# Performance work log

Measured on AMD Instinct MI355X. Metric: run time of the kernel, lower is better.

## Reference

```python
import jax, jax.numpy as jnp
import numpy as np

B, S, H, NH = 4, 2048, 1024, 16
HS = H // NH  # head size 64


def setup_inputs() -> dict:
    key = jax.random.key(0)
    ks = jax.random.split(key, 12)
    inv = 1.0 / np.sqrt(H)
    d = {
        "query": jax.random.normal(ks[0], (B, S, H), jnp.float32),
        "key": jax.random.normal(ks[1], (B, S, H), jnp.float32),
        "value": jax.random.normal(ks[2], (B, S, H), jnp.float32),
        "causal_mask": jnp.tril(jnp.ones((S, S), dtype=bool)),
        "Wq": jax.random.uniform(ks[3], (H, H), jnp.float32, -inv, inv),
        "bq": jax.random.uniform(ks[4], (H,), jnp.float32, -inv, inv),
        "Wk": jax.random.uniform(ks[5], (H, H), jnp.float32, -inv, inv),
        "bk": jax.random.uniform(ks[6], (H,), jnp.float32, -inv, inv),
        "Wv": jax.random.uniform(ks[7], (H, H), jnp.float32, -inv, inv),
        "bv": jax.random.uniform(ks[8], (H,), jnp.float32, -inv, inv),
        "Wo": jax.random.uniform(ks[9], (H, H), jnp.float32, -inv, inv),
        "bo": jax.random.uniform(ks[10], (H,), jnp.float32, -inv, inv),
    }
    return d


def reference(query, key, value, causal_mask, Wq, bq, Wk, bk, Wv, bv, Wo, bo):
    # Linear projections (torch Linear: x @ W.T + b)
    q = query @ Wq.T + bq
    k = key @ Wk.T + bk
    v = value @ Wv.T + bv
    # [B, NH, S, HS]
    q = q.reshape(B, S, NH, HS).transpose(0, 2, 1, 3)
    k = k.reshape(B, S, NH, HS).transpose(0, 2, 1, 3)
    v = v.reshape(B, S, NH, HS).transpose(0, 2, 1, 3)
    scores = jnp.einsum("bhqd,bhkd->bhqk", q, k) / jnp.sqrt(jnp.float32(HS))
    scores = jnp.where(causal_mask[None, None, :, :], scores, -jnp.inf)
    attn = jax.nn.softmax(scores, axis=-1)
    ctx = jnp.einsum("bhqk,bhkd->bhqd", attn, v)
    ctx = ctx.transpose(0, 2, 1, 3).reshape(B, S, H)
    return ctx @ Wo.T + bo
```

## Files before the change

### kernel.cpp

```cpp
#include <hip/hip_runtime.h>
#include <hip/hip_bf16.h>
#include <math.h>

#define B_  4
#define S_  2048
#define H_  1024
#define NH_ 16
#define HS_ 64

typedef __attribute__((ext_vector_type(8))) short bf16x8;
typedef __attribute__((ext_vector_type(4))) short bf16x4;
typedef __attribute__((ext_vector_type(4))) float f32x4;

__device__ __forceinline__ short f2bf(float f) {
    unsigned u = __builtin_bit_cast(unsigned, f);
    u += 0x7FFFu + ((u >> 16) & 1u);
    return (short)(u >> 16);
}

typedef __attribute__((address_space(3))) void lds_void;
typedef const __attribute__((address_space(1))) void g_void;
__device__ __forceinline__ void gl_lds16(const void* g, void* l) {
    __builtin_amdgcn_global_load_lds((g_void*)g, (lds_void*)l, 16, 0, 0);
}


__global__ __launch_bounds__(256) void cvt_all_k(
    const float* __restrict__ a0, const float* __restrict__ a1,
    const float* __restrict__ a2, const float* __restrict__ w0,
    const float* __restrict__ w1, const float* __restrict__ w2,
    const float* __restrict__ w3,
    short* o0, short* o1, short* o2, short* o3, short* o4, short* o5, short* o6)
{
    const int y = blockIdx.y;
    const float* ins[7]  = {a0, a1, a2, w0, w1, w2, w3};
    short*       outs[7] = {o0, o1, o2, o3, o4, o5, o6};
    const int n8 = (y < 3) ? (int)((size_t)B_ * S_ * H_ / 8) : (int)((size_t)H_ * H_ / 8);
    const int i = blockIdx.x * 256 + threadIdx.x;
    if (i >= n8) return;
    const float4* p = (const float4*)ins[y] + (size_t)i * 2;
    float4 a = p[0], b = p[1];
    bf16x8 o;
    o[0] = f2bf(a.x); o[1] = f2bf(a.y); o[2] = f2bf(a.z); o[3] = f2bf(a.w);
    o[4] = f2bf(b.x); o[5] = f2bf(b.y); o[6] = f2bf(b.z); o[7] = f2bf(b.w);
    *(bf16x8*)(outs[y] + (size_t)i * 8) = o;
}

__device__ __forceinline__ void gemm_core(
    const short* __restrict__ A, const short* __restrict__ W,
    int m0, int n0, short* As, short* Ws, f32x4 acc[4][4])
{
    const int tid  = threadIdx.x;
    const int w    = tid >> 6;
    const int lane = tid & 63;
    const int l15  = lane & 15;
    const int q4   = lane >> 4;
    const int wm   = w >> 1;
    const int wn   = w & 1;
    const int K    = 1024;
    const int swz  = l15 & 7;

    const char* Abase = (const char*)A + (size_t)m0 * K * 2;
    const char* Wbase = (const char*)W + (size_t)n0 * K * 2;

    #pragma unroll
    for (int mi = 0; mi < 4; ++mi)
        #pragma unroll
        for (int ni = 0; ni < 4; ++ni)
            acc[mi][ni] = (f32x4){0.f, 0.f, 0.f, 0.f};

    for (int k0 = 0; k0 < K; k0 += 64) {
        __syncthreads();
        #pragma unroll
        for (int t = 0; t < 4; ++t) {
            const int ob  = t * 4096 + w * 1024;
            const int idx = t * 256 + w * 64 + lane;
            const int row = idx >> 3;
            const int sc  = (idx & 7) ^ (row & 7);
            gl_lds16(Abase + (size_t)row * (K * 2) + k0 * 2 + sc * 16, (char*)As + ob);
            gl_lds16(Wbase + (size_t)row * (K * 2) + k0 * 2 + sc * 16, (char*)Ws + ob);
        }
        __syncthreads();

        #pragma unroll
        for (int kh = 0; kh < 2; ++kh) {
            bf16x8 af[4], bf[4];
            #pragma unroll
            for (int mi = 0; mi < 4; ++mi)
                af[mi] = *(const bf16x8*)(As + (wm * 64 + mi * 16 + l15) * 64
                                             + (((kh * 4 + q4) ^ swz) * 8));
            #pragma unroll
            for (int ni = 0; ni < 4; ++ni)
                bf[ni] = *(const bf16x8*)(Ws + (wn * 64 + ni * 16 + l15) * 64
                                             + (((kh * 4 + q4) ^ swz) * 8));
            #pragma unroll
            for (int mi = 0; mi < 4; ++mi)
                #pragma unroll
                for (int ni = 0; ni < 4; ++ni)
                    acc[mi][ni] = __builtin_amdgcn_mfma_f32_16x16x32_bf16(
                        af[mi], bf[ni], acc[mi][ni], 0, 0, 0);
        }
    }
}

__global__ __launch_bounds__(256) void gemm_proj_k(
    const short* __restrict__ Aq, const short* __restrict__ Wqb,
    const float* __restrict__ bq, short* __restrict__ qb,
    const short* __restrict__ Ak, const short* __restrict__ Wkb,
    const float* __restrict__ bk, short* __restrict__ kb,
    const short* __restrict__ Wvb, const short* __restrict__ Av,
    const float* __restrict__ bv, short* __restrict__ vtb)
{
    __shared__ short As[128 * 64];
    __shared__ short Ws[128 * 64];

    const int z = blockIdx.z;
    const short *A, *W; const float* bias; short* out;
    if (z == 0)      { A = Aq;  W = Wqb; bias = bq; out = qb;  }
    else if (z == 1) { A = Ak;  W = Wkb; bias = bk; out = kb;  }
    else             { A = Wvb; W = Av;  bias = bv; out = vtb; }
    const int m0 = (z == 2 ? blockIdx.y : blockIdx.x) * 128;
    const int n0 = (z == 2 ? blockIdx.x : blockIdx.y) * 128;

    f32x4 acc[4][4];
    gemm_core(A, W, m0, n0, As, Ws, acc);

    const int tid  = threadIdx.x;
    const int w    = tid >> 6;
    const int lane = tid & 63;
    const int l15  = lane & 15;
    const int q4   = lane >> 4;
    const int wm   = w >> 1;
    const int wn   = w & 1;

    #pragma unroll
    for (int mi = 0; mi < 4; ++mi) {
        #pragma unroll
        for (int r = 0; r < 4; ++r) {
            const int m = m0 + wm * 64 + mi * 16 + q4 * 4 + r;
            #pragma unroll
            for (int ni = 0; ni < 4; ++ni) {
                const int n = n0 + wn * 64 + ni * 16 + l15;
                const float v = acc[mi][ni][r] + bias[z == 2 ? m : n];
                if (z != 2) {
                    const int b = m >> 11, s = m & (S_ - 1);
                    const int h = n >> 6,  d = n & (HS_ - 1);
                    out[(((size_t)b * NH_ + h) * S_ + s) * HS_ + d] = f2bf(v);
                } else {
                    const int b = n >> 11, s = n & (S_ - 1);
                    const int h = m >> 6,  d = m & (HS_ - 1);
                    out[(((size_t)b * NH_ + h) * HS_ + d) * S_ + s] = f2bf(v);
                }
            }
        }
    }
}

__global__ __launch_bounds__(256) void gemm_out_k(
    const short* __restrict__ A, const short* __restrict__ W,
    const float* __restrict__ bias, float* __restrict__ Cout)
{
    __shared__ short As[128 * 64];
    __shared__ short Ws[128 * 64];
    const int m0 = blockIdx.x * 128;
    const int n0 = blockIdx.y * 128;

    f32x4 acc[4][4];
    gemm_core(A, W, m0, n0, As, Ws, acc);

    const int tid  = threadIdx.x;
    const int w    = tid >> 6;
    const int lane = tid & 63;
    const int l15  = lane & 15;
    const int q4   = lane >> 4;
    const int wm   = w >> 1;
    const int wn   = w & 1;

    #pragma unroll
    for (int mi = 0; mi < 4; ++mi)
        #pragma unroll
        for (int r = 0; r < 4; ++r) {
            const int m = m0 + wm * 64 + mi * 16 + q4 * 4 + r;
            #pragma unroll
            for (int ni = 0; ni < 4; ++ni) {
                const int n = n0 + wn * 64 + ni * 16 + l15;
                Cout[(size_t)m * H_ + n] = acc[mi][ni][r] + bias[n];
            }
        }
}

#define PPAD_ 72

__global__ __launch_bounds__(256) void attn_mfma(
    const short* __restrict__ Q, const short* __restrict__ K,
    const short* __restrict__ VT, short* __restrict__ O)
{
    __shared__ short Ks[2][64 * 64];
    __shared__ short Vt[2][64 * 64];
    __shared__ short Pl[4][32 * PPAD_];

    const int tid  = threadIdx.x;
    const int w    = tid >> 6;
    const int lane = tid & 63;
    const int l15  = lane & 15;
    const int q4   = lane >> 4;
    const int swz  = l15 & 7;
    const int bh   = blockIdx.y;
    const size_t base = (size_t)bh * S_ * HS_;
    const int b = bh >> 4;
    const int h = bh & 15;
    const float SC = 0.125f * 1.44269504f;

#define STAGE_KV(slot_, kt_)                                                      \
    do {                                                                          \
        _Pragma("unroll")                                                         \
        for (int t = 0; t < 2; ++t) {                                             \
            const int ob  = (slot_) * 8192 + t * 4096 + w * 1024;                 \
            const int idx = t * 256 + w * 64 + lane;        \
            const int r   = idx >> 3;                                             \
            const int sc  = (idx & 7) ^ (r & 7);          \
            gl_lds16(K + base + (size_t)((kt_) * 64 + r) * HS_ + sc * 8,          \
                     (char*)Ks + ob);                                             \
            gl_lds16(VT + base + (size_t)r * S_ + (kt_) * 64 + sc * 8,            \
                     (char*)Vt + ob);                                             \
        }                                                                         \
    } while (0)

    #pragma unroll 1
    for (int pass = 0; pass < 2; ++pass) {
        const int qt = pass ? (15 - blockIdx.x) : blockIdx.x;
        const int ktmax = 2 * qt + 1;

        STAGE_KV(0, 0);

        bf16x8 aQ[2][2];
        #pragma unroll
        for (int mi = 0; mi < 2; ++mi) {
            const int qrow = qt * 128 + w * 32 + mi * 16 + l15;
            #pragma unroll
            for (int kh = 0; kh < 2; ++kh)
                aQ[mi][kh] = *(const bf16x8*)(Q + base + (size_t)qrow * HS_ + kh * 32 + q4 * 8);
        }

        f32x4 accO[2][4];
        float lsum[2];
        #pragma unroll
        for (int mi = 0; mi < 2; ++mi) {
            #pragma unroll
            for (int db = 0; db < 4; ++db) accO[mi][db] = (f32x4){0.f, 0.f, 0.f, 0.f};
            lsum[mi] = 0.f;
        }

        __syncthreads();

        for (int kt = 0; kt <= ktmax; ++kt) {
            const int cur = kt & 1;
            if (kt < ktmax) STAGE_KV(cur ^ 1, kt + 1);

            f32x4 sbT[2][4];
            const short* KsBase = &Ks[cur][0];
            __builtin_amdgcn_s_setprio(1);
            #pragma unroll
            for (int nb = 0; nb < 4; ++nb) {
                const short* krow = KsBase + (nb * 16 + l15) * 64;
                bf16x8 k0 = *(const bf16x8*)(krow + ((q4 ^ swz) * 8));
                bf16x8 k1 = *(const bf16x8*)(krow + (((4 + q4) ^ swz) * 8));
                #pragma unroll
                for (int mi = 0; mi < 2; ++mi) {
                    f32x4 a = (f32x4){0.f, 0.f, 0.f, 0.f};
                    a = __builtin_amdgcn_mfma_f32_16x16x32_bf16(k0, aQ[mi][0], a, 0, 0, 0);
                    a = __builtin_amdgcn_mfma_f32_16x16x32_bf16(k1, aQ[mi][1], a, 0, 0, 0);
                    sbT[mi][nb] = a;
                }
            }
            __builtin_amdgcn_s_setprio(0);

            const bool need_mask = (kt >= 2 * qt);
            #pragma unroll
            for (int mi = 0; mi < 2; ++mi) {
                const int qrow = qt * 128 + w * 32 + mi * 16 + l15;
                #pragma unroll
                for (int nb = 0; nb < 4; ++nb) {
                    bf16x4 pk;
                    #pragma unroll
                    for (int r = 0; r < 4; ++r) {
                        float sv = sbT[mi][nb][r];
                        if (need_mask) {
                            const int kj = kt * 64 + nb * 16 + q4 * 4 + r;
                            if (kj > qrow) sv = -INFINITY;
                        }
                        const float p = exp2f(sv * SC);
                        lsum[mi] += p;
                        pk[r] = f2bf(p);
                    }
                    *(bf16x4*)&Pl[w][(mi * 16 + l15) * PPAD_ + nb * 16 + q4 * 4] = pk;
                }
            }

            bf16x8 aP[2][2];
            #pragma unroll
            for (int mi = 0; mi < 2; ++mi)
                #pragma unroll
                for (int kh = 0; kh < 2; ++kh)
                    aP[mi][kh] = *(const bf16x8*)(&Pl[w][(mi * 16 + l15) * PPAD_ + kh * 32 + q4 * 8]);
            const short* VtBase = &Vt[cur][0];
            __builtin_amdgcn_s_setprio(1);
            #pragma unroll
            for (int db = 0; db < 4; ++db) {
                const short* vrow = VtBase + (db * 16 + l15) * 64;
                bf16x8 v0 = *(const bf16x8*)(vrow + ((q4 ^ swz) * 8));
                bf16x8 v1 = *(const bf16x8*)(vrow + (((4 + q4) ^ swz) * 8));
                #pragma unroll
                for (int mi = 0; mi < 2; ++mi) {
                    accO[mi][db] = __builtin_amdgcn_mfma_f32_16x16x32_bf16(aP[mi][0], v0, accO[mi][db], 0, 0, 0);
                    accO[mi][db] = __builtin_amdgcn_mfma_f32_16x16x32_bf16(aP[mi][1], v1, accO[mi][db], 0, 0, 0);
                }
            }
            __builtin_amdgcn_s_setprio(0);

            __syncthreads();
        }

        #pragma unroll
        for (int mi = 0; mi < 2; ++mi) {
            float ls = lsum[mi];
            ls += __shfl_xor(ls, 16);
            ls += __shfl_xor(ls, 32);
            #pragma unroll
            for (int r = 0; r < 4; ++r) {
                const float inv = 1.f / __shfl(ls, q4 * 4 + r);
                const int orow = qt * 128 + w * 32 + mi * 16 + q4 * 4 + r;
                short* op = O + ((size_t)(b * S_ + orow)) * H_ + h * HS_;
                #pragma unroll
                for (int db = 0; db < 4; ++db)
                    op[db * 16 + l15] = f2bf(accO[mi][db][r] * inv);
            }
        }
    }
#undef STAGE_KV
}

extern "C" void kernel_launch(void* const* d_in, const int* in_sizes, int n_in,
                              void* d_out, int out_size, void* d_ws, size_t ws_size,
                              hipStream_t stream)
{
    const float* query = (const float*)d_in[0];
    const float* key   = (const float*)d_in[1];
    const float* value = (const float*)d_in[2];
    const float* Wq = (const float*)d_in[4];
    const float* bq = (const float*)d_in[5];
    const float* Wk = (const float*)d_in[6];
    const float* bk = (const float*)d_in[7];
    const float* Wv = (const float*)d_in[8];
    const float* bv = (const float*)d_in[9];
    const float* Wo = (const float*)d_in[10];
    const float* bo = (const float*)d_in[11];
    float* out = (float*)d_out;

    const size_t EA = (size_t)B_ * S_ * H_;
    const size_t EW = (size_t)H_ * H_;

    short* Aq  = (short*)d_ws;
    short* Ak  = Aq  + EA;
    short* Av  = Ak  + EA;
    short* Wqb = Av  + EA;
    short* Wkb = Wqb + EW;
    short* Wvb = Wkb + EW;
    short* Wob = Wvb + EW;
    short* qb  = Wob + EW;
    short* kb  = qb  + EA;
    short* vtb = kb  + EA;
    short* cb  = vtb + EA;

    const int M = B_ * S_;

    cvt_all_k<<<dim3((int)(EA / 8 / 256), 7), 256, 0, stream>>>(
        query, key, value, Wq, Wk, Wv, Wo,
        Aq, Ak, Av, Wqb, Wkb, Wvb, Wob);

    gemm_proj_k<<<dim3(M / 128, H_ / 128, 3), 256, 0, stream>>>(
        Aq, Wqb, bq, qb, Ak, Wkb, bk, kb, Wvb, Av, bv, vtb);

    attn_mfma<<<dim3(S_ / 256, B_ * NH_), 256, 0, stream>>>(qb, kb, vtb, cb);

    gemm_out_k<<<dim3(M / 128, H_ / 128), 256, 0, stream>>>(cb, Wob, bo, out);
}
```

Baseline: 380.6 us.

## Keep softmax probabilities in registers and fold the score scale into Q

The softmax scale (1/sqrt(d)·log2e) is now folded into the Q projection epilogue, so the attention loop applies a raw v_exp_f32 with no multiply. The P matrix no longer round-trips through LDS: probabilities are packed to bf16 in registers with v_cvt_pk_bf16_f32. The V-tile reads are reordered into 4-element halves so the MFMA k-index permutation matches the register-resident P layout. This removes LDS writes and reads plus the conversion overhead per tile, at the cost of bf16 rounding of the pre-scaled Q and less efficient narrower LDS reads for V.

```diff
diff --git a/kernel.cpp b/kernel.cpp
--- a/kernel.cpp
+++ b/kernel.cpp
@@ -9,8 +9,11 @@
 #define HS_ 64
 
 typedef __attribute__((ext_vector_type(8))) short bf16x8;
-typedef __attribute__((ext_vector_type(4))) short bf16x4;
+typedef __attribute__((ext_vector_type(4))) short s16x4;
 typedef __attribute__((ext_vector_type(4))) float f32x4;
+typedef __attribute__((ext_vector_type(4))) unsigned u32x4;
+
+#define QSCALE_ (0.125f * 1.44269504f)
 
 __device__ __forceinline__ short f2bf(float f) {
     unsigned u = __builtin_bit_cast(unsigned, f);
@@ -141,7 +144,8 @@
             #pragma unroll
             for (int ni = 0; ni < 4; ++ni) {
                 const int n = n0 + wn * 64 + ni * 16 + l15;
-                const float v = acc[mi][ni][r] + bias[z == 2 ? m : n];
+                float v = acc[mi][ni][r] + bias[z == 2 ? m : n];
+                if (z == 0) v *= QSCALE_;
                 if (z != 2) {
                     const int b = m >> 11, s = m & (S_ - 1);
                     const int h = n >> 6,  d = n & (HS_ - 1);
@@ -189,15 +193,12 @@
         }
 }
 
-#define PPAD_ 72
-
 __global__ __launch_bounds__(256) void attn_mfma(
     const short* __restrict__ Q, const short* __restrict__ K,
     const short* __restrict__ VT, short* __restrict__ O)
 {
     __shared__ short Ks[2][64 * 64];
     __shared__ short Vt[2][64 * 64];
-    __shared__ short Pl[4][32 * PPAD_];
 
     const int tid  = threadIdx.x;
     const int w    = tid >> 6;
@@ -209,7 +210,6 @@
     const size_t base = (size_t)bh * S_ * HS_;
     const int b = bh >> 4;
     const int h = bh & 15;
-    const float SC = 0.125f * 1.44269504f;
 
 #define STAGE_KV(slot_, kt_)                                                      \
     do {                                                                          \
@@ -257,7 +257,7 @@
             const int cur = kt & 1;
             if (kt < ktmax) STAGE_KV(cur ^ 1, kt + 1);
 
-            f32x4 sbT[2][4];
+            f32x4 sT[2][4];
             const short* KsBase = &Ks[cur][0];
             __builtin_amdgcn_s_setprio(1);
             #pragma unroll
@@ -270,50 +270,66 @@
                     f32x4 a = (f32x4){0.f, 0.f, 0.f, 0.f};
                     a = __builtin_amdgcn_mfma_f32_16x16x32_bf16(k0, aQ[mi][0], a, 0, 0, 0);
                     a = __builtin_amdgcn_mfma_f32_16x16x32_bf16(k1, aQ[mi][1], a, 0, 0, 0);
-                    sbT[mi][nb] = a;
+                    sT[mi][nb] = a;
                 }
             }
             __builtin_amdgcn_s_setprio(0);
 
-            const bool need_mask = (kt >= 2 * qt);
+            if (kt >= 2 * qt) {
+                #pragma unroll
+                for (int mi = 0; mi < 2; ++mi) {
+                    const int qrow = qt * 128 + w * 32 + mi * 16 + l15;
+                    #pragma unroll
+                    for (int nb = 0; nb < 4; ++nb)
+                        #pragma unroll
+                        for (int r = 0; r < 4; ++r) {
+                            const int kj = kt * 64 + nb * 16 + q4 * 4 + r;
+                            if (kj > qrow) sT[mi][nb][r] = -INFINITY;
+                        }
+                }
+            }
+
+            bf16x8 aP[2][2];
             #pragma unroll
             for (int mi = 0; mi < 2; ++mi) {
-                const int qrow = qt * 128 + w * 32 + mi * 16 + l15;
-                #pragma unroll
-                for (int nb = 0; nb < 4; ++nb) {
-                    bf16x4 pk;
+                float p[4][4];
+                #pragma unroll
+                for (int nb = 0; nb < 4; ++nb)
                     #pragma unroll
                     for (int r = 0; r < 4; ++r) {
-                        float sv = sbT[mi][nb][r];
-                        if (need_mask) {
-                            const int kj = kt * 64 + nb * 16 + q4 * 4 + r;
-                            if (kj > qrow) sv = -INFINITY;
-                        }
-                        const float p = exp2f(sv * SC);
-                        lsum[mi] += p;
-                        pk[r] = f2bf(p);
+                        float pv;
+                        asm("v_exp_f32 %0, %1" : "=v"(pv) : "v"(sT[mi][nb][r]));
+                        lsum[mi] += pv;
+                        p[nb][r] = pv;
                     }
-                    *(bf16x4*)&Pl[w][(mi * 16 + l15) * PPAD_ + nb * 16 + q4 * 4] = pk;
+                #pragma unroll
+                for (int hf = 0; hf < 2; ++hf) {
+                    unsigned w0, w1, w2, w3;
+                    asm("v_cvt_pk_bf16_f32 %0, %1, %2" : "=v"(w0) : "v"(p[2*hf][0]),   "v"(p[2*hf][1]));
+                    asm("v_cvt_pk_bf16_f32 %0, %1, %2" : "=v"(w1) : "v"(p[2*hf][2]),   "v"(p[2*hf][3]));
+                    asm("v_cvt_pk_bf16_f32 %0, %1, %2" : "=v"(w2) : "v"(p[2*hf+1][0]), "v"(p[2*hf+1][1]));
+                    asm("v_cvt_pk_bf16_f32 %0, %1, %2" : "=v"(w3) : "v"(p[2*hf+1][2]), "v"(p[2*hf+1][3]));
+                    u32x4 pw; pw[0] = w0; pw[1] = w1; pw[2] = w2; pw[3] = w3;
+                    aP[mi][hf] = __builtin_bit_cast(bf16x8, pw);
                 }
             }
 
-            bf16x8 aP[2][2];
-            #pragma unroll
-            for (int mi = 0; mi < 2; ++mi)
-                #pragma unroll
-                for (int kh = 0; kh < 2; ++kh)
-                    aP[mi][kh] = *(const bf16x8*)(&Pl[w][(mi * 16 + l15) * PPAD_ + kh * 32 + q4 * 8]);
             const short* VtBase = &Vt[cur][0];
             __builtin_amdgcn_s_setprio(1);
             #pragma unroll
             for (int db = 0; db < 4; ++db) {
                 const short* vrow = VtBase + (db * 16 + l15) * 64;
-                bf16x8 v0 = *(const bf16x8*)(vrow + ((q4 ^ swz) * 8));
-                bf16x8 v1 = *(const bf16x8*)(vrow + (((4 + q4) ^ swz) * 8));
-                #pragma unroll
-                for (int mi = 0; mi < 2; ++mi) {
-                    accO[mi][db] = __builtin_amdgcn_mfma_f32_16x16x32_bf16(aP[mi][0], v0, accO[mi][db], 0, 0, 0);
-                    accO[mi][db] = __builtin_amdgcn_mfma_f32_16x16x32_bf16(aP[mi][1], v1, accO[mi][db], 0, 0, 0);
+                #pragma unroll
+                for (int hf = 0; hf < 2; ++hf) {
+                    const int lc0 = 4 * hf + (q4 >> 1);
+                    const int lc1 = lc0 + 2;
+                    s16x4 vlo = *(const s16x4*)(vrow + ((lc0 ^ swz) * 8) + 4 * (q4 & 1));
+                    s16x4 vhi = *(const s16x4*)(vrow + ((lc1 ^ swz) * 8) + 4 * (q4 & 1));
+                    bf16x8 vf = __builtin_shufflevector(vlo, vhi, 0, 1, 2, 3, 4, 5, 6, 7);
+                    #pragma unroll
+                    for (int mi = 0; mi < 2; ++mi)
+                        accO[mi][db] = __builtin_amdgcn_mfma_f32_16x16x32_bf16(
+                            aP[mi][hf], vf, accO[mi][db], 0, 0, 0);
                 }
             }
             __builtin_amdgcn_s_setprio(0);
```

Measured after the change: 349.7 us. 8.1% less time.
